# Performance work log

Hardware: AMD Instinct MI355X
Metric: run time of the kernel (lower is better)

## Reference

```python
import jax, jax.numpy as jnp
import numpy as np

ALPHA, BETA, GAMMA, DELTA = 1.0, 1.0, 0.5, 0.3


def setup_inputs() -> dict:
    key = jax.random.key(0)
    k1, k2, k3, k4, k5 = jax.random.split(key, 5)
    B, R = 1024, 192
    return {
        "position_updates": jax.random.uniform(k1, (B, R, 2), dtype=jnp.float32),
        "size_updates": jax.random.uniform(k2, (B, R, 2), dtype=jnp.float32),
        "target_positions": jax.random.uniform(k3, (B, R, 2), dtype=jnp.float32),
        "target_sizes": jax.random.uniform(k4, (B, R, 2), dtype=jnp.float32),
        "adjacency_matrix": jax.random.randint(k5, (1, R, R), 0, 2, dtype=jnp.int32),
    }


def reference(position_updates, size_updates, target_positions, target_sizes, adjacency_matrix):
    # MSE terms
    position_loss = jnp.mean((position_updates - target_positions) ** 2)
    size_loss = jnp.mean((size_updates - target_sizes) ** 2)

    R = position_updates.shape[1]
    triu = jnp.triu(jnp.ones((R, R), dtype=bool), k=1)  # pairs i<j

    # Pairwise overlap penalty, vectorized over all (i, j) pairs.
    x = position_updates[..., 0]  # [B, R]
    y = position_updates[..., 1]
    w = size_updates[..., 0]
    h = size_updates[..., 1]
    # [B, R, R] broadcasted pairwise intersections
    ow = jnp.clip(jnp.minimum((x + w)[:, :, None], (x + w)[:, None, :])
                  - jnp.maximum(x[:, :, None], x[:, None, :]), 0)
    oh = jnp.clip(jnp.minimum((y + h)[:, :, None], (y + h)[:, None, :])
                  - jnp.maximum(y[:, :, None], y[:, None, :]), 0)
    overlap_area = ow * oh  # [B, R, R]
    overlap_penalty = jnp.sum(jnp.where(triu, overlap_area.mean(axis=0), 0.0))

    # Adjacency loss: distance between centers of adjacent rooms (adj from batch 0)
    centers = position_updates + size_updates / 2  # [B, R, 2]
    cx, cy = centers[..., 0], centers[..., 1]
    dx = cx[:, :, None] - cx[:, None, :]
    dy = cy[:, :, None] - cy[:, None, :]
    sq = dx * dx + dy * dy  # [B, R, R]
    adj_mask = triu & (adjacency_matrix[0] > 0)  # [R, R]
    dist = jnp.sqrt(jnp.where(adj_mask[None, :, :], sq, 1.0))  # safe sqrt
    adjacency_loss = jnp.sum(jnp.where(adj_mask, dist.mean(axis=0), 0.0))

    total_loss = (ALPHA * position_loss + BETA * size_loss
                  + GAMMA * overlap_penalty + DELTA * adjacency_loss)
    return (total_loss, position_loss, size_loss, overlap_penalty, adjacency_loss)
```

## Files before the change

kernel.cpp:

```cpp
#include <hip/hip_runtime.h>

#define R 192
#define BATCH 1024
#define TILE 16
#define NT (R / TILE)

__global__ void init_ws_kernel(float* __restrict__ ws) {
    int t = threadIdx.x;
    if (t < 4) ws[t] = 0.0f;
}

__global__ __launch_bounds__(256) void floorplan_main_kernel(
    const float* __restrict__ pos,
    const float* __restrict__ siz,
    const float* __restrict__ tpos,
    const float* __restrict__ tsiz,
    const int*   __restrict__ adj,
    float* __restrict__ ws)
{
    __shared__ float sx[R], sy[R], sw[R], sh[R];
    __shared__ float wsum[4][4];

    const int b   = blockIdx.x;
    const int tid = threadIdx.x;

    const float* pb  = pos  + (size_t)b * (R * 2);
    const float* sb  = siz  + (size_t)b * (R * 2);
    const float* tpb = tpos + (size_t)b * (R * 2);
    const float* tsb = tsiz + (size_t)b * (R * 2);

    float mse_p = 0.0f, mse_s = 0.0f;

    for (int idx = tid; idx < R * 2; idx += 256) {
        float p  = pb[idx];
        float s  = sb[idx];
        float dp = p - tpb[idx];
        float ds = s - tsb[idx];
        mse_p += dp * dp;
        mse_s += ds * ds;
        int r = idx >> 1;
        if (idx & 1) { sy[r] = p; sh[r] = s; }
        else         { sx[r] = p; sw[r] = s; }
    }
    __syncthreads();

    float ov = 0.0f, ad = 0.0f;
    const int li = tid >> 4;
    const int lj = tid & 15;

    for (int ti = 0; ti < NT; ++ti) {
        const int   i   = ti * TILE + li;
        const float xi  = sx[i], yi = sy[i], wi = sw[i], hi = sh[i];
        const float xiw = xi + wi;
        const float yih = yi + hi;
        const float cxi = xi + 0.5f * wi;
        const float cyi = yi + 0.5f * hi;

        for (int tj = ti; tj < NT; ++tj) {
            const int j = tj * TILE + lj;
            if (i < j) {
                const float xj = sx[j], yj = sy[j], wj = sw[j], hj = sh[j];
                float ow = fminf(xiw, xj + wj) - fmaxf(xi, xj);
                float oh = fminf(yih, yj + hj) - fmaxf(yi, yj);
                ow = fmaxf(ow, 0.0f);
                oh = fmaxf(oh, 0.0f);
                ov += ow * oh;
                if (adj[i * R + j] > 0) {
                    float dx = cxi - (xj + 0.5f * wj);
                    float dy = cyi - (yj + 0.5f * hj);
                    ad += sqrtf(dx * dx + dy * dy);
                }
            }
        }
    }

    for (int off = 32; off > 0; off >>= 1) {
        mse_p += __shfl_down(mse_p, off);
        mse_s += __shfl_down(mse_s, off);
        ov    += __shfl_down(ov, off);
        ad    += __shfl_down(ad, off);
    }
    const int wid  = tid >> 6;
    const int lane = tid & 63;
    if (lane == 0) {
        wsum[wid][0] = mse_p;
        wsum[wid][1] = mse_s;
        wsum[wid][2] = ov;
        wsum[wid][3] = ad;
    }
    __syncthreads();
    if (tid < 4) {
        float v = wsum[0][tid] + wsum[1][tid] + wsum[2][tid] + wsum[3][tid];
        atomicAdd(&ws[tid], v);
    }
}

__global__ void finalize_kernel(const float* __restrict__ ws, float* __restrict__ out) {
    if (threadIdx.x == 0 && blockIdx.x == 0) {
        const float invN = 1.0f / (float)(BATCH * R * 2);
        const float invB = 1.0f / (float)BATCH;
        float pos_loss  = ws[0] * invN;
        float size_loss = ws[1] * invN;
        float overlap   = ws[2] * invB;
        float adjl      = ws[3] * invB;
        out[0] = pos_loss + size_loss + 0.5f * overlap + 0.3f * adjl;
        out[1] = pos_loss;
        out[2] = size_loss;
        out[3] = overlap;
        out[4] = adjl;
    }
}

extern "C" void kernel_launch(void* const* d_in, const int* in_sizes, int n_in,
                              void* d_out, int out_size, void* d_ws, size_t ws_size,
                              hipStream_t stream) {
    const float* pos  = (const float*)d_in[0];
    const float* siz  = (const float*)d_in[1];
    const float* tpos = (const float*)d_in[2];
    const float* tsiz = (const float*)d_in[3];
    const int*   adj  = (const int*)d_in[4];
    float* ws  = (float*)d_ws;
    float* out = (float*)d_out;

    hipLaunchKernelGGL(init_ws_kernel, dim3(1), dim3(64), 0, stream, ws);
    hipLaunchKernelGGL(floorplan_main_kernel, dim3(BATCH), dim3(256), 0, stream,
                       pos, siz, tpos, tsiz, adj, ws);
    hipLaunchKernelGGL(finalize_kernel, dim3(1), dim3(1), 0, stream, ws, out);
}
```

Measured before the change: 103.3 us.

## Pack adjacency into bitmask, split pair tiles across two blocks, branchless inner loop

A pre-pass kernel turns the triu-masked adjacency matrix into a 192x6-word bitmask using wavefront ballots, and each main block copies it into shared memory instead of reading int adjacency from global memory per pair. The main grid doubles, with blockIdx.y interleaving the column tiles between two blocks per batch element. Room data is packed as float4 in shared memory and the inner loop becomes branchless: it computes every pair and masks the results, using the fast hardware sqrt. This adds redundant staging of the room data and bitmask in each of the two blocks, plus wasted sqrt work on non-adjacent pairs.

```diff
diff --git a/kernel.cpp b/kernel.cpp
--- a/kernel.cpp
+++ b/kernel.cpp
@@ -4,10 +4,23 @@
 #define BATCH 1024
 #define TILE 16
 #define NT (R / TILE)
+#define NBITWORDS (R * 6)
 
-__global__ void init_ws_kernel(float* __restrict__ ws) {
-    int t = threadIdx.x;
-    if (t < 4) ws[t] = 0.0f;
+
+__global__ __launch_bounds__(256) void build_mask_kernel(
+    const int* __restrict__ adj, float* __restrict__ ws)
+{
+    unsigned int* wsbits = (unsigned int*)(ws + 4);
+    const int e = blockIdx.x * 256 + threadIdx.x;
+    if (e < 4) ws[e] = 0.0f;
+    if (e >= R * R) return;
+    const int i = e / R;
+    const int j = e - i * R;
+    const bool pred = (adj[e] > 0) && (j > i);
+    const unsigned long long m = __ballot(pred);
+    const int lane = e & 63;
+    if (lane == 0)  wsbits[e >> 5] = (unsigned int)m;
+    if (lane == 32) wsbits[e >> 5] = (unsigned int)(m >> 32);
 }
 
 __global__ __launch_bounds__(256) void floorplan_main_kernel(
@@ -15,62 +28,71 @@
     const float* __restrict__ siz,
     const float* __restrict__ tpos,
     const float* __restrict__ tsiz,
-    const int*   __restrict__ adj,
     float* __restrict__ ws)
 {
-    __shared__ float sx[R], sy[R], sw[R], sh[R];
+    __shared__ float4 room[R];
+    __shared__ unsigned int sadj[NBITWORDS];
     __shared__ float wsum[4][4];
 
     const int b   = blockIdx.x;
+    const int sel = blockIdx.y;
     const int tid = threadIdx.x;
 
-    const float* pb  = pos  + (size_t)b * (R * 2);
-    const float* sb  = siz  + (size_t)b * (R * 2);
-    const float* tpb = tpos + (size_t)b * (R * 2);
-    const float* tsb = tsiz + (size_t)b * (R * 2);
+    const float2* pb  = (const float2*)(pos  + (size_t)b * (R * 2));
+    const float2* sb  = (const float2*)(siz  + (size_t)b * (R * 2));
+    const float2* tpb = (const float2*)(tpos + (size_t)b * (R * 2));
+    const float2* tsb = (const float2*)(tsiz + (size_t)b * (R * 2));
+    const unsigned int* wsbits = (const unsigned int*)(ws + 4);
 
     float mse_p = 0.0f, mse_s = 0.0f;
 
-    for (int idx = tid; idx < R * 2; idx += 256) {
-        float p  = pb[idx];
-        float s  = sb[idx];
-        float dp = p - tpb[idx];
-        float ds = s - tsb[idx];
-        mse_p += dp * dp;
-        mse_s += ds * ds;
-        int r = idx >> 1;
-        if (idx & 1) { sy[r] = p; sh[r] = s; }
-        else         { sx[r] = p; sw[r] = s; }
+    if (tid < R) {
+        float2 p  = pb[tid];
+        float2 s  = sb[tid];
+        float2 tp = tpb[tid];
+        float2 ts = tsb[tid];
+        float dpx = p.x - tp.x, dpy = p.y - tp.y;
+        float dsx = s.x - ts.x, dsy = s.y - ts.y;
+        mse_p = dpx * dpx + dpy * dpy;
+        mse_s = dsx * dsx + dsy * dsy;
+        room[tid] = make_float4(p.x, p.y, s.x, s.y);
     }
+    for (int w = tid; w < NBITWORDS; w += 256) sadj[w] = wsbits[w];
     __syncthreads();
+
+    if (sel != 0) { mse_p = 0.0f; mse_s = 0.0f; }
 
     float ov = 0.0f, ad = 0.0f;
     const int li = tid >> 4;
     const int lj = tid & 15;
 
     for (int ti = 0; ti < NT; ++ti) {
-        const int   i   = ti * TILE + li;
-        const float xi  = sx[i], yi = sy[i], wi = sw[i], hi = sh[i];
-        const float xiw = xi + wi;
-        const float yih = yi + hi;
-        const float cxi = xi + 0.5f * wi;
-        const float cyi = yi + 0.5f * hi;
+        const int   i  = ti * TILE + li;
+        const float4 ri = room[i];
+        const float xi  = ri.x, yi = ri.y;
+        const float xiw = ri.x + ri.z;
+        const float yih = ri.y + ri.w;
+        const float cxi = fmaf(0.5f, ri.z, ri.x);
+        const float cyi = fmaf(0.5f, ri.w, ri.y);
+        const unsigned int* rowbits = &sadj[i * 6];
 
-        for (int tj = ti; tj < NT; ++tj) {
+        for (int tj = ti + sel; tj < NT; tj += 2) {
             const int j = tj * TILE + lj;
-            if (i < j) {
-                const float xj = sx[j], yj = sy[j], wj = sw[j], hj = sh[j];
-                float ow = fminf(xiw, xj + wj) - fmaxf(xi, xj);
-                float oh = fminf(yih, yj + hj) - fmaxf(yi, yj);
-                ow = fmaxf(ow, 0.0f);
-                oh = fmaxf(oh, 0.0f);
-                ov += ow * oh;
-                if (adj[i * R + j] > 0) {
-                    float dx = cxi - (xj + 0.5f * wj);
-                    float dy = cyi - (yj + 0.5f * hj);
-                    ad += sqrtf(dx * dx + dy * dy);
-                }
-            }
+            const float4 rj = room[j];
+            float ow = fminf(xiw, rj.x + rj.z) - fmaxf(xi, rj.x);
+            float oh = fminf(yih, rj.y + rj.w) - fmaxf(yi, rj.y);
+            ow = fmaxf(ow, 0.0f);
+            oh = fmaxf(oh, 0.0f);
+            float area = ow * oh;
+            ov += (i < j) ? area : 0.0f;
+
+            unsigned int wbits = rowbits[tj >> 1];
+            unsigned int bit = (wbits >> (((tj & 1) << 4) + lj)) & 1u;
+            float dx = cxi - fmaf(0.5f, rj.z, rj.x);
+            float dy = cyi - fmaf(0.5f, rj.w, rj.y);
+            float sq = fmaf(dx, dx, dy * dy);
+            float d  = __builtin_amdgcn_sqrtf(sq);
+            ad += bit ? d : 0.0f;
         }
     }
 
@@ -122,8 +144,9 @@
     float* ws  = (float*)d_ws;
     float* out = (float*)d_out;
 
-    hipLaunchKernelGGL(init_ws_kernel, dim3(1), dim3(64), 0, stream, ws);
-    hipLaunchKernelGGL(floorplan_main_kernel, dim3(BATCH), dim3(256), 0, stream,
-                       pos, siz, tpos, tsiz, adj, ws);
+    hipLaunchKernelGGL(build_mask_kernel, dim3((R * R + 255) / 256), dim3(256), 0, stream,
+                       adj, ws);
+    hipLaunchKernelGGL(floorplan_main_kernel, dim3(BATCH, 2), dim3(256), 0, stream,
+                       pos, siz, tpos, tsiz, ws);
     hipLaunchKernelGGL(finalize_kernel, dim3(1), dim3(1), 0, stream, ws, out);
 }
```

New measurement: 101.1 us. 1.02x faster.
